# Kernel optimization log

Measured on AMD Instinct MI355X. Metric: run time of the kernel, lower is better.

## Reference

```python
import jax, jax.numpy as jnp
import numpy as np

EPS = 1e-12  # F.normalize default eps


def _wn_weight(v, g):
    # torch weight_norm(dim=0) on Conv1d weight [out, in, 1]: w = g * v / ||v||_rows
    norm = jnp.sqrt(jnp.sum(v * v, axis=1, keepdims=True))
    return v * (g[:, None] / norm)


def _l2norm(x):
    n = jnp.sqrt(jnp.sum(x * x, axis=-1, keepdims=True))
    return x / jnp.maximum(n, EPS)


def setup_inputs() -> dict:
    key = jax.random.key(0)
    ks = jax.random.split(key, 4)
    B, D, T = 16, 1024, 4096
    CD, CS = 8, 1024
    return {
        "z": jax.random.normal(ks[0], (B, D, T), dtype=jnp.float32),
        "in_proj_v": jax.random.normal(ks[1], (CD, D), dtype=jnp.float32) * 0.02,
        "in_proj_g": jnp.ones((CD,), dtype=jnp.float32),
        "in_proj_b": jnp.zeros((CD,), dtype=jnp.float32),
        "out_proj_v": jax.random.normal(ks[2], (D, CD), dtype=jnp.float32) * 0.02,
        "out_proj_g": jnp.ones((D,), dtype=jnp.float32),
        "out_proj_b": jnp.zeros((D,), dtype=jnp.float32),
        "codebook": jax.random.normal(ks[3], (CS, CD), dtype=jnp.float32),
    }


def reference(z, in_proj_v, in_proj_g, in_proj_b, out_proj_v, out_proj_g, out_proj_b, codebook):
    B, D, T = z.shape
    CD = codebook.shape[1]

    # in_proj: 1x1 weight-normed conv == per-timestep linear
    w_in = _wn_weight(in_proj_v, in_proj_g)            # [CD, D]
    z_e = jnp.einsum('od,bdt->bot', w_in, z) + in_proj_b[None, :, None]  # [B, CD, T]

    # decode_latents: cosine-distance nearest neighbor in normalized space
    enc = jnp.transpose(z_e, (0, 2, 1)).reshape(B * T, CD)  # (b t) d
    enc_n = _l2norm(enc)
    cb_n = _l2norm(codebook)
    # dist = |e|^2 - 2 e.c + |c|^2 over normalized vectors
    dist = (jnp.sum(enc_n * enc_n, axis=1, keepdims=True)
            - 2.0 * enc_n @ cb_n.T
            + jnp.sum(cb_n * cb_n, axis=1)[None, :])       # [B*T, CS]
    indices = jnp.argmax(-dist, axis=1).reshape(B, T)      # [B, T]
    z_q = jnp.transpose(codebook[indices], (0, 2, 1))      # [B, CD, T] (un-normalized codebook gather)

    # losses (reduce over dims [1,2] -> per-batch)
    sg = jax.lax.stop_gradient
    commitment_loss = jnp.mean((z_e - sg(z_q)) ** 2, axis=(1, 2))
    codebook_loss = jnp.mean((z_q - sg(z_e)) ** 2, axis=(1, 2))

    # straight-through
    z_q_st = z_e + sg(z_q - z_e)

    w_out = _wn_weight(out_proj_v, out_proj_g)          # [D, CD]
    out = jnp.einsum('dc,bct->bdt', w_out, z_q_st) + out_proj_b[None, :, None]
    return out, commitment_loss, codebook_loss, indices, z_e
```

## Files before the change

### kernel.cpp

```cpp
#include <hip/hip_runtime.h>
#include <math.h>

#define BB 16
#define DD 1024
#define TT 4096
#define CD 8
#define CS 1024

#define OFF_LOSS_C 67108864
#define OFF_LOSS_B 67108880
#define OFF_IDX    67108896
#define OFF_ZE     67174432

#define WS_WIN  0
#define WS_WOUT 8192
#define WS_CBN  16384
#define WS_CS   24576

#define TILE_T 128

__global__ __launch_bounds__(256) void prep_kernel(
    const float* __restrict__ in_v,
    const float* __restrict__ in_g,
    const float* __restrict__ out_v,
    const float* __restrict__ out_g,
    const float* __restrict__ cb,
    float* __restrict__ ws)
{
    int bid = blockIdx.x, tid = threadIdx.x;
    if (bid < 8) {
        __shared__ float red[256];
        __shared__ float ssc;
        int o = bid;
        float p = 0.f;
        for (int k = tid; k < DD; k += 256) { float v = in_v[o*DD + k]; p += v*v; }
        red[tid] = p; __syncthreads();
        for (int s = 128; s > 0; s >>= 1) { if (tid < s) red[tid] += red[tid+s]; __syncthreads(); }
        if (tid == 0) ssc = in_g[o] / sqrtf(red[0]);
        __syncthreads();
        float scale = ssc;
        for (int d = tid; d < DD; d += 256)
            ws[WS_WIN + d*CD + o] = in_v[o*DD + d] * scale;
    } else if (bid < 12) {
        int d = (bid - 8) * 256 + tid;
        float v[CD]; float ssq = 0.f;
        #pragma unroll
        for (int c = 0; c < CD; ++c) { v[c] = out_v[d*CD + c]; ssq += v[c]*v[c]; }
        float s = out_g[d] / sqrtf(ssq);
        #pragma unroll
        for (int c = 0; c < CD; ++c) ws[WS_WOUT + d*CD + c] = v[c]*s;
    } else {
        int c = (bid - 12) * 256 + tid;
        double* csh = (double*)(ws + WS_CS);
        float v[CD]; float ssq = 0.f;
        #pragma unroll
        for (int j = 0; j < CD; ++j) { v[j] = cb[c*CD + j]; ssq += v[j]*v[j]; }
        float n = fmaxf(sqrtf(ssq), 1e-12f);
        double sq = 0.0;
        #pragma unroll
        for (int j = 0; j < CD; ++j) {
            float e = v[j] / n;
            ws[WS_CBN + c*CD + j] = e;
            sq = fma((double)e, (double)e, sq);
        }
        csh[c] = 0.5 * sq;
    }
}

__global__ __launch_bounds__(512, 4) void fused_kernel(
    const float* __restrict__ z,
    const float* __restrict__ in_b,
    const float* __restrict__ cb,
    const float* __restrict__ out_b,
    const float* __restrict__ ws,
    float* __restrict__ outb)
{
    __shared__ float  zpart[8][CD][TILE_T];
    __shared__ float  ze_s[CD][TILE_T];
    __shared__ float  nrm_s[TILE_T];
    __shared__ double best_s[4][TILE_T];
    __shared__ int    bidx_s[4][TILE_T];
    __shared__ __align__(16) float zq_s[CD][TILE_T];

    int tid  = threadIdx.x;
    int b    = blockIdx.y;
    int t0   = blockIdx.x * TILE_T;
    int lane = tid & 63;
    int wv   = __builtin_amdgcn_readfirstlane(tid >> 6);

    {
        const float* zp = z + ((size_t)(b*DD + wv*128)) * TT + t0 + lane*2;
        const float* w  = ws + WS_WIN + wv*128*CD;
        float2 acc[CD];
        #pragma unroll
        for (int o = 0; o < CD; ++o) acc[o] = make_float2(0.f, 0.f);
        #pragma unroll 8
        for (int j = 0; j < 128; ++j) {
            float2 zv = *(const float2*)(zp + (size_t)j * TT);
            #pragma unroll
            for (int o = 0; o < CD; ++o) {
                float wo = w[j*CD + o];
                acc[o].x = fmaf(wo, zv.x, acc[o].x);
                acc[o].y = fmaf(wo, zv.y, acc[o].y);
            }
        }
        #pragma unroll
        for (int o = 0; o < CD; ++o)
            *(float2*)&zpart[wv][o][lane*2] = acc[o];
    }
    __syncthreads();

    #pragma unroll
    for (int p = tid; p < CD*TILE_T; p += 512) {
        int o = p >> 7, t = p & 127;
        float v = (((zpart[0][o][t] + zpart[1][o][t]) + (zpart[2][o][t] + zpart[3][o][t]))
                 + ((zpart[4][o][t] + zpart[5][o][t]) + (zpart[6][o][t] + zpart[7][o][t])))
                 + in_b[o];
        ze_s[o][t] = v;
        outb[OFF_ZE + ((size_t)(b*CD + o)) * TT + t0 + t] = v;
    }
    __syncthreads();
    if (tid < TILE_T) {
        float ssq = 0.f;
        #pragma unroll
        for (int o = 0; o < CD; ++o) { float vv = ze_s[o][tid]; ssq = fmaf(vv, vv, ssq); }
        nrm_s[tid] = fmaxf(sqrtf(ssq), 1e-12f);
    }
    __syncthreads();

    {
        int t  = tid & 127;
        int ck = __builtin_amdgcn_readfirstlane(tid >> 7);
        float nr = nrm_s[t];
        double en[CD];
        #pragma unroll
        for (int o = 0; o < CD; ++o) en[o] = (double)(ze_s[o][t] / nr);
        const float*  cbn = ws + WS_CBN;
        const double* csh = (const double*)(ws + WS_CS);
        int c0 = ck * 256;
        double best = -1.0e300; int bi = c0;
        for (int c = c0; c < c0 + 256; ++c) {
            float cr[CD];
            *(float4*)&cr[0] = *(const float4*)(cbn + c*CD);
            *(float4*)&cr[4] = *(const float4*)(cbn + c*CD + 4);
            double dot = 0.0;
            #pragma unroll
            for (int o = 0; o < CD; ++o) dot = fma((double)cr[o], en[o], dot);
            double score = dot - csh[c];
            if (score > best) { best = score; bi = c; }
        }
        best_s[ck][t] = best; bidx_s[ck][t] = bi;
    }
    __syncthreads();

    if (tid < TILE_T) {
        int t = tid;
        double best = best_s[0][t]; int bi = bidx_s[0][t];
        #pragma unroll
        for (int k = 1; k < 4; ++k) {
            if (best_s[k][t] > best) { best = best_s[k][t]; bi = bidx_s[k][t]; }
        }
        outb[OFF_IDX + b*TT + t0 + t] = (float)bi;

        float q[CD];
        *(float4*)&q[0] = *(const float4*)(cb + bi*CD);
        *(float4*)&q[4] = *(const float4*)(cb + bi*CD + 4);
        #pragma unroll
        for (int o = 0; o < CD; ++o) zq_s[o][t] = q[o];

        float l = 0.f;
        #pragma unroll
        for (int o = 0; o < CD; ++o) { float d = ze_s[o][t] - q[o]; l = fmaf(d, d, l); }
        #pragma unroll
        for (int off = 32; off > 0; off >>= 1) l += __shfl_down(l, off, 64);
        if (lane == 0) {
            float s = l * (1.0f / (CD * TT));
            atomicAdd(outb + OFF_LOSS_C + b, s);
            atomicAdd(outb + OFF_LOSS_B + b, s);
        }
    }
    __syncthreads();

    {
        int tq = tid & 31;
        int dg = tid >> 5;
        float4 qv[CD];
        #pragma unroll
        for (int o = 0; o < CD; ++o) qv[o] = *(const float4*)&zq_s[o][tq*4];

        size_t obase = (size_t)b * DD * TT + t0 + tq*4;
        const float4* wv4 = (const float4*)(ws + WS_WOUT);
        #pragma unroll 4
        for (int i = 0; i < 64; ++i) {
            int d = dg*64 + i;
            float wr[CD];
            *(float4*)&wr[0] = wv4[2*d];
            *(float4*)&wr[4] = wv4[2*d + 1];
            float bbv = out_b[d];
            float4 r = make_float4(bbv, bbv, bbv, bbv);
            #pragma unroll
            for (int o = 0; o < CD; ++o) {
                float wo = wr[o];
                r.x = fmaf(wo, qv[o].x, r.x);
                r.y = fmaf(wo, qv[o].y, r.y);
                r.z = fmaf(wo, qv[o].z, r.z);
                r.w = fmaf(wo, qv[o].w, r.w);
            }
            *(float4*)(outb + obase + (size_t)d * TT) = r;
        }
    }
}

extern "C" void kernel_launch(void* const* d_in, const int* in_sizes, int n_in,
                              void* d_out, int out_size, void* d_ws, size_t ws_size,
                              hipStream_t stream) {
    const float* z     = (const float*)d_in[0];
    const float* in_v  = (const float*)d_in[1];
    const float* in_g  = (const float*)d_in[2];
    const float* in_b  = (const float*)d_in[3];
    const float* out_v = (const float*)d_in[4];
    const float* out_g = (const float*)d_in[5];
    const float* out_b = (const float*)d_in[6];
    const float* cb    = (const float*)d_in[7];
    float* ws  = (float*)d_ws;
    float* out = (float*)d_out;

    hipMemsetAsync(out + OFF_LOSS_C, 0, 32 * sizeof(float), stream);

    prep_kernel<<<16, 256, 0, stream>>>(in_v, in_g, out_v, out_g, cb, ws);
    fused_kernel<<<dim3(TT/TILE_T, BB), 512, 0, stream>>>(z, in_b, cb, out_b, ws, out);
}
```

Before: 558.0 us.

## Halve time tile to 64, use 256-thread blocks, add nontemporal output stores

Shrinks the time tile from 128 to 64 and the block from 512 to 256 threads, so each wave reduces 256 input channels with scalar loads instead of 128 channels with float2 loads, and each wave scans its own quarter of the codebook. The output projection now interleaves channel rows across thread groups and writes through nontemporal stores, aiming to keep the large output stream out of cache. Together these double the block count to improve occupancy and load balance on the memory-bound kernel. The cost is more per-thread serial work in the reduction and narrower loads per lane.

```diff
diff --git a/kernel.cpp b/kernel.cpp
--- a/kernel.cpp
+++ b/kernel.cpp
@@ -17,7 +17,9 @@
 #define WS_CBN  16384
 #define WS_CS   24576
 
-#define TILE_T 128
+#define TILE_T 64
+
+typedef float vfloat4 __attribute__((ext_vector_type(4)));
 
 __global__ __launch_bounds__(256) void prep_kernel(
     const float* __restrict__ in_v,
@@ -67,7 +69,7 @@
     }
 }
 
-__global__ __launch_bounds__(512, 4) void fused_kernel(
+__global__ __launch_bounds__(256, 4) void fused_kernel(
     const float* __restrict__ z,
     const float* __restrict__ in_b,
     const float* __restrict__ cb,
@@ -75,7 +77,7 @@
     const float* __restrict__ ws,
     float* __restrict__ outb)
 {
-    __shared__ float  zpart[8][CD][TILE_T];
+    __shared__ float  zpart[4][CD][TILE_T];
     __shared__ float  ze_s[CD][TILE_T];
     __shared__ float  nrm_s[TILE_T];
     __shared__ double best_s[4][TILE_T];
@@ -85,37 +87,31 @@
     int tid  = threadIdx.x;
     int b    = blockIdx.y;
     int t0   = blockIdx.x * TILE_T;
-    int lane = tid & 63;
+    int tl   = tid & 63;
     int wv   = __builtin_amdgcn_readfirstlane(tid >> 6);
 
     {
-        const float* zp = z + ((size_t)(b*DD + wv*128)) * TT + t0 + lane*2;
-        const float* w  = ws + WS_WIN + wv*128*CD;
-        float2 acc[CD];
-        #pragma unroll
-        for (int o = 0; o < CD; ++o) acc[o] = make_float2(0.f, 0.f);
-        #pragma unroll 8
-        for (int j = 0; j < 128; ++j) {
-            float2 zv = *(const float2*)(zp + (size_t)j * TT);
+        const float* zp = z + ((size_t)(b*DD + wv*256)) * TT + t0 + tl;
+        const float* w  = ws + WS_WIN + wv*256*CD;
+        float acc[CD];
+        #pragma unroll
+        for (int o = 0; o < CD; ++o) acc[o] = 0.f;
+        #pragma unroll 16
+        for (int j = 0; j < 256; ++j) {
+            float zv = zp[(size_t)j * TT];
             #pragma unroll
-            for (int o = 0; o < CD; ++o) {
-                float wo = w[j*CD + o];
-                acc[o].x = fmaf(wo, zv.x, acc[o].x);
-                acc[o].y = fmaf(wo, zv.y, acc[o].y);
-            }
-        }
-        #pragma unroll
-        for (int o = 0; o < CD; ++o)
-            *(float2*)&zpart[wv][o][lane*2] = acc[o];
+            for (int o = 0; o < CD; ++o) acc[o] = fmaf(w[j*CD + o], zv, acc[o]);
+        }
+        #pragma unroll
+        for (int o = 0; o < CD; ++o) zpart[wv][o][tl] = acc[o];
     }
     __syncthreads();
 
     #pragma unroll
-    for (int p = tid; p < CD*TILE_T; p += 512) {
-        int o = p >> 7, t = p & 127;
-        float v = (((zpart[0][o][t] + zpart[1][o][t]) + (zpart[2][o][t] + zpart[3][o][t]))
-                 + ((zpart[4][o][t] + zpart[5][o][t]) + (zpart[6][o][t] + zpart[7][o][t])))
-                 + in_b[o];
+    for (int p = tid; p < CD*TILE_T; p += 256) {
+        int o = p >> 6, t = p & 63;
+        float v = in_b[o] + ((zpart[0][o][t] + zpart[1][o][t]) +
+                             (zpart[2][o][t] + zpart[3][o][t]));
         ze_s[o][t] = v;
         outb[OFF_ZE + ((size_t)(b*CD + o)) * TT + t0 + t] = v;
     }
@@ -129,15 +125,14 @@
     __syncthreads();
 
     {
-        int t  = tid & 127;
-        int ck = __builtin_amdgcn_readfirstlane(tid >> 7);
+        int t = tl;
         float nr = nrm_s[t];
         double en[CD];
         #pragma unroll
         for (int o = 0; o < CD; ++o) en[o] = (double)(ze_s[o][t] / nr);
         const float*  cbn = ws + WS_CBN;
         const double* csh = (const double*)(ws + WS_CS);
-        int c0 = ck * 256;
+        int c0 = wv * 256;
         double best = -1.0e300; int bi = c0;
         for (int c = c0; c < c0 + 256; ++c) {
             float cr[CD];
@@ -149,7 +144,7 @@
             double score = dot - csh[c];
             if (score > best) { best = score; bi = c; }
         }
-        best_s[ck][t] = best; bidx_s[ck][t] = bi;
+        best_s[wv][t] = best; bidx_s[wv][t] = bi;
     }
     __syncthreads();
 
@@ -173,7 +168,7 @@
         for (int o = 0; o < CD; ++o) { float d = ze_s[o][t] - q[o]; l = fmaf(d, d, l); }
         #pragma unroll
         for (int off = 32; off > 0; off >>= 1) l += __shfl_down(l, off, 64);
-        if (lane == 0) {
+        if (tid == 0) {
             float s = l * (1.0f / (CD * TT));
             atomicAdd(outb + OFF_LOSS_C + b, s);
             atomicAdd(outb + OFF_LOSS_B + b, s);
@@ -182,8 +177,8 @@
     __syncthreads();
 
     {
-        int tq = tid & 31;
-        int dg = tid >> 5;
+        int tq = tid & 15;
+        int dg = tid >> 4;
         float4 qv[CD];
         #pragma unroll
         for (int o = 0; o < CD; ++o) qv[o] = *(const float4*)&zq_s[o][tq*4];
@@ -192,12 +187,12 @@
         const float4* wv4 = (const float4*)(ws + WS_WOUT);
         #pragma unroll 4
         for (int i = 0; i < 64; ++i) {
-            int d = dg*64 + i;
+            int d = i*16 + dg;
             float wr[CD];
             *(float4*)&wr[0] = wv4[2*d];
             *(float4*)&wr[4] = wv4[2*d + 1];
             float bbv = out_b[d];
-            float4 r = make_float4(bbv, bbv, bbv, bbv);
+            vfloat4 r = { bbv, bbv, bbv, bbv };
             #pragma unroll
             for (int o = 0; o < CD; ++o) {
                 float wo = wr[o];
@@ -206,7 +201,7 @@
                 r.z = fmaf(wo, qv[o].z, r.z);
                 r.w = fmaf(wo, qv[o].w, r.w);
             }
-            *(float4*)(outb + obase + (size_t)d * TT) = r;
+            __builtin_nontemporal_store(r, (vfloat4*)(outb + obase + (size_t)d * TT));
         }
     }
 }
@@ -225,8 +220,8 @@
     float* ws  = (float*)d_ws;
     float* out = (float*)d_out;
 
-    hipMemsetAsync(out + OFF_LOSS_C, 0, 32 * sizeof(float), stream);
+    (void)hipMemsetAsync(out + OFF_LOSS_C, 0, 32 * sizeof(float), stream);
 
     prep_kernel<<<16, 256, 0, stream>>>(in_v, in_g, out_v, out_g, cb, ws);
-    fused_kernel<<<dim3(TT/TILE_T, BB), 512, 0, stream>>>(z, in_b, cb, out_b, ws, out);
+    fused_kernel<<<dim3(TT/TILE_T, BB), 256, 0, stream>>>(z, in_b, cb, out_b, ws, out);
 }
```

New measurement: 546.9 us. 1.02x faster.
